# Performance work log

Hardware: AMD Instinct MI355X
Metric: run time of the kernel (lower is better)

Reference implementation:

```python
import jax, jax.numpy as jnp
import numpy as np

B = 16384
F = 128   # num_features
H = 128   # hidden_dim
E = 32    # embedding_dim


def setup_inputs() -> dict:
    key = jax.random.key(0)
    k_x, k_w1, k_b1, k_w2, k_b2 = jax.random.split(key, 5)
    # Per-feature params stacked along feature axis.
    # Layer 1: Linear(1 -> H): weight [F, H] (in_dim==1 squeezed), bias [F, H]
    # Layer 2: Linear(H -> E): weight [F, H, E], bias [F, E]
    # Torch default init: U(-1/sqrt(fan_in), 1/sqrt(fan_in))
    w1 = jax.random.uniform(k_w1, (F, H), jnp.float32, -1.0, 1.0)          # fan_in=1
    b1 = jax.random.uniform(k_b1, (F, H), jnp.float32, -1.0, 1.0)
    bound2 = 1.0 / np.sqrt(H)
    w2 = jax.random.uniform(k_w2, (F, H, E), jnp.float32, -bound2, bound2)
    b2 = jax.random.uniform(k_b2, (F, E), jnp.float32, -bound2, bound2)
    x = jax.random.normal(k_x, (B, F), jnp.float32)
    return {"x": x, "w1": w1, "b1": b1, "w2": w2, "b2": b2}


def reference(x, w1, b1, w2, b2):
    # Fused over features: broadcast-mul replaces K=1 matmuls,
    # single batched GEMM replaces per-feature second Linear.
    h = jax.nn.relu(x[:, :, None] * w1[None] + b1[None])   # [B, F, H]
    out = jnp.einsum('bfh,fhe->bfe', h, w2) + b2[None]      # [B, F, E]
    return out.reshape(x.shape[0], F * E)                   # concat along last dim
```

## Files before the change

### kernel.cpp

```cpp
#include <hip/hip_runtime.h>
#include <math.h>

#define B_N 16384
#define F_N 128
#define H_N 128
#define E_N 32
#define ROWS (H_N + 1)

typedef float f4v __attribute__((ext_vector_type(4)));

__global__ __launch_bounds__(128) void build_tables(
    const float* __restrict__ w1, const float* __restrict__ b1,
    const float* __restrict__ w2, const float* __restrict__ b2,
    float* __restrict__ ts_out, float* __restrict__ tab)
{
    __shared__ float w1s[H_N], b1s[H_N], ts[H_N];
    __shared__ int   hidx[H_N];
    __shared__ float w2s[H_N * E_N];
    __shared__ float dA[H_N * E_N];
    __shared__ float dC[H_N * E_N];
    __shared__ float baseA[4 * E_N], baseC[4 * E_N];
    __shared__ float gtA[4 * E_N], gtC[4 * E_N];

    const int f   = blockIdx.x;
    const int tid = threadIdx.x;

    float w1v = w1[f * H_N + tid];
    float b1v = b1[f * H_N + tid];
    w1s[tid] = w1v;
    b1s[tid] = b1v;
    ts[tid]   = (w1v != 0.0f) ? (-b1v / w1v) : INFINITY;
    hidx[tid] = tid;

    {
        const float4* src = (const float4*)(w2 + (size_t)f * H_N * E_N);
        float4*       dst = (float4*)w2s;
        #pragma unroll
        for (int it = 0; it < 8; ++it) dst[it * 128 + tid] = src[it * 128 + tid];
    }
    __syncthreads();

    for (int k = 2; k <= H_N; k <<= 1) {
        for (int j = k >> 1; j > 0; j >>= 1) {
            int ixj = tid ^ j;
            if (ixj > tid) {
                float a = ts[tid], bv = ts[ixj];
                bool up = ((tid & k) == 0);
                bool sw = up ? (a > bv) : (a < bv);
                if (sw) {
                    int ia = hidx[tid];
                    ts[tid] = bv; ts[ixj] = a;
                    hidx[tid] = hidx[ixj]; hidx[ixj] = ia;
                }
            }
            __syncthreads();
        }
    }

    ts_out[f * H_N + tid] = ts[tid];

    const int e = tid & 31;
    const int g = tid >> 5;

    #pragma unroll 4
    for (int jj = 0; jj < 32; ++jj) {
        int   j   = g * 32 + jj;
        int   p   = hidx[j];
        float w1h = w1s[p], b1h = b1s[p];
        float w2v = w2s[p * E_N + e];
        float s   = (w1h > 0.f) ? 1.f : ((w1h < 0.f) ? -1.f : 0.f);
        dA[j * E_N + e] = s * w1h * w2v;
        dC[j * E_N + e] = s * b1h * w2v;
    }
    {
        float pA = 0.f, pC = 0.f;
        #pragma unroll 4
        for (int hh = 0; hh < 32; ++hh) {
            int   h   = g * 32 + hh;
            float w1h = w1s[h], b1h = b1s[h];
            float w2v = w2s[h * E_N + e];
            if (w1h < 0.f) {
                pA = fmaf(w1h, w2v, pA);
                pC = fmaf(b1h, w2v, pC);
            } else if (w1h == 0.f && b1h > 0.f) {
                pC = fmaf(b1h, w2v, pC);
            }
        }
        baseA[g * E_N + e] = pA;
        baseC[g * E_N + e] = pC;
    }

    {
        float aA = 0.f, aC = 0.f;
        for (int jj = 0; jj < 32; ++jj) {
            int idx = (g * 32 + jj) * E_N + e;
            aA += dA[idx]; dA[idx] = aA;
            aC += dC[idx]; dC[idx] = aC;
        }
        gtA[g * E_N + e] = aA;
        gtC[g * E_N + e] = aC;
    }
    __syncthreads();

    float offA = baseA[e] + baseA[E_N + e] + baseA[2 * E_N + e] + baseA[3 * E_N + e];
    float offC = baseC[e] + baseC[E_N + e] + baseC[2 * E_N + e] + baseC[3 * E_N + e]
               + b2[f * E_N + e];
    for (int gg = 0; gg < g; ++gg) {
        offA += gtA[gg * E_N + e];
        offC += gtC[gg * E_N + e];
    }

    const size_t base = (size_t)f * ROWS * 64;
    if (g == 0) {
        tab[base + e]      = offA;
        tab[base + 32 + e] = offC;
    }
    #pragma unroll 4
    for (int jj = 0; jj < 32; ++jj) {
        int j = g * 32 + jj;
        tab[base + (size_t)(j + 1) * 64 + e]      = offA + dA[j * E_N + e];
        tab[base + (size_t)(j + 1) * 64 + 32 + e] = offC + dC[j * E_N + e];
    }
}

#define FH 32
#define NB 64

__global__ __launch_bounds__(256, 4) void apply_tables(
    const float* __restrict__ x, const float* __restrict__ ts,
    const float* __restrict__ tab, float* __restrict__ out)
{
    __shared__ float lds_t[FH * ROWS];
    __shared__ float xs[NB * FH];
    __shared__ int   los[NB * FH];

    const int tid = threadIdx.x;

    const unsigned bid  = blockIdx.x;
    const unsigned work = (bid & 7u) * 128u + (bid >> 3);
    const int b0 = (int)(work & 255u) * NB;
    const int f0 = (int)(work >> 8)  * FH;

    {
        const float4* src = (const float4*)(ts + (size_t)f0 * H_N);
        #pragma unroll
        for (int it = 0; it < 4; ++it) {
            int    vi  = it * 256 + tid;
            float4 v   = src[vi];
            int    idx = vi * 4;
            int    fl  = idx >> 7;
            int    j   = idx & 127;
            float* dst = &lds_t[fl * ROWS + j];
            dst[0] = v.x; dst[1] = v.y; dst[2] = v.z; dst[3] = v.w;
        }
    }
    {
        #pragma unroll
        for (int it = 0; it < 2; ++it) {
            int vi = it * 256 + tid;
            int bl = vi >> 3;
            int fq = (vi & 7) * 4;
            float4 v = *(const float4*)(x + (size_t)(b0 + bl) * F_N + f0 + fq);
            *(float4*)(&xs[bl * FH + fq]) = v;
        }
    }
    __syncthreads();

    {
        const int fa = tid & 31;
        const int rg = tid >> 5;
        const float* tloc = &lds_t[fa * ROWS];
        float xv[8];
        int   lo[8], hi[8];
        #pragma unroll
        for (int j = 0; j < 8; ++j) {
            xv[j] = xs[(rg * 8 + j) * FH + fa];
            lo[j] = 0; hi[j] = H_N;
        }
        #pragma unroll
        for (int s = 0; s < 7; ++s) {
            #pragma unroll
            for (int j = 0; j < 8; ++j) {
                int  mid = (lo[j] + hi[j]) >> 1;
                bool lt  = tloc[mid] < xv[j];
                lo[j] = lt ? mid + 1 : lo[j];
                hi[j] = lt ? hi[j] : mid;
            }
        }
        #pragma unroll
        for (int j = 0; j < 8; ++j) los[(rg * 8 + j) * FH + fa] = lo[j];
    }
    __syncthreads();

    const int fl = tid >> 3;
    const int eq = tid & 7;
    const int fg = f0 + fl;
    const float* tb = tab + (size_t)fg * ROWS * 64 + eq * 4;
    float*       op = out + (size_t)b0 * (F_N * E_N) + (size_t)fg * E_N + eq * 4;

    #pragma unroll 4
    for (int r = 0; r < NB; ++r) {
        int   lo = los[r * FH + fl];
        float xv = xs[r * FH + fl];
        const float* row = tb + (size_t)lo * 64;
        f4v a4 = *(const f4v*)(row);
        f4v c4 = *(const f4v*)(row + 32);
        f4v o;
        o.x = fmaf(xv, a4.x, c4.x);
        o.y = fmaf(xv, a4.y, c4.y);
        o.z = fmaf(xv, a4.z, c4.z);
        o.w = fmaf(xv, a4.w, c4.w);
        __builtin_nontemporal_store(o, (f4v*)(op + (size_t)r * (F_N * E_N)));
    }
}

__global__ __launch_bounds__(256) void direct_kernel(
    const float* __restrict__ x, const float* __restrict__ w1,
    const float* __restrict__ b1, const float* __restrict__ w2,
    const float* __restrict__ b2, float* __restrict__ out)
{
    __shared__ float w1s[H_N], b1s[H_N], b2s[E_N];
    __shared__ float w2s[H_N * E_N];
    const int f   = blockIdx.y;
    const int tid = threadIdx.x;
    if (tid < H_N) { w1s[tid] = w1[f * H_N + tid]; b1s[tid] = b1[f * H_N + tid]; }
    for (int i = tid; i < H_N * E_N; i += 256) w2s[i] = w2[(size_t)f * H_N * E_N + i];
    if (tid < E_N) b2s[tid] = b2[f * E_N + tid];
    __syncthreads();

    const int b  = blockIdx.x * 256 + tid;
    float xv = x[(size_t)b * F_N + f];
    float acc[E_N];
    #pragma unroll
    for (int e = 0; e < E_N; ++e) acc[e] = b2s[e];
    for (int h = 0; h < H_N; ++h) {
        float hv = fmaxf(fmaf(xv, w1s[h], b1s[h]), 0.f);
        #pragma unroll
        for (int e = 0; e < E_N; ++e) acc[e] = fmaf(hv, w2s[h * E_N + e], acc[e]);
    }
    float* op = out + (size_t)b * (F_N * E_N) + (size_t)f * E_N;
    #pragma unroll
    for (int e = 0; e < E_N; e += 4)
        *(float4*)(op + e) = make_float4(acc[e], acc[e + 1], acc[e + 2], acc[e + 3]);
}

extern "C" void kernel_launch(void* const* d_in, const int* in_sizes, int n_in,
                              void* d_out, int out_size, void* d_ws, size_t ws_size,
                              hipStream_t stream) {
    const float* x  = (const float*)d_in[0];
    const float* w1 = (const float*)d_in[1];
    const float* b1 = (const float*)d_in[2];
    const float* w2 = (const float*)d_in[3];
    const float* b2 = (const float*)d_in[4];
    float* out = (float*)d_out;

    const size_t n_ts  = (size_t)F_N * H_N;
    const size_t n_tab = (size_t)F_N * ROWS * 64;
    const size_t need  = (n_ts + n_tab) * sizeof(float);

    if (ws_size >= need) {
        float* ts  = (float*)d_ws;
        float* tab = ts + n_ts;
        build_tables<<<dim3(F_N), dim3(128), 0, stream>>>(w1, b1, w2, b2, ts, tab);
        apply_tables<<<dim3((B_N / NB) * (F_N / FH)), dim3(256), 0, stream>>>(x, ts, tab, out);
    } else {
        direct_kernel<<<dim3(B_N / 256, F_N), dim3(256), 0, stream>>>(x, w1, b1, w2, b2, out);
    }
}
```

Baseline: 287.7 us.

## Interleave A/C table rows, shuffle search results, halve batch tile

The table layout now interleaves A and C coefficients in groups of four, so each lane reads one contiguous 32-byte span instead of two separate 16-byte loads. apply_tables drops the shared x and segment-index buffers and one barrier. Each thread now binary-searches 4 rows itself and broadcasts the results with wave shuffles. The batch tile shrinks from 64 to 32 rows and occupancy is raised to 8 blocks. This trades LDS traffic and a sync for more blocks, a repeated ts load per block, and shuffle overhead.

```diff
diff --git a/kernel.cpp b/kernel.cpp
--- a/kernel.cpp
+++ b/kernel.cpp
@@ -8,6 +8,8 @@
 #define ROWS (H_N + 1)
 
 typedef float f4v __attribute__((ext_vector_type(4)));
+
+__device__ __forceinline__ int eidxA(int e) { return ((e >> 2) << 3) | (e & 3); }
 
 __global__ __launch_bounds__(128) void build_tables(
     const float* __restrict__ w1, const float* __restrict__ b1,
@@ -111,35 +113,34 @@
     }
 
     const size_t base = (size_t)f * ROWS * 64;
+    const int    eA   = eidxA(e);
     if (g == 0) {
-        tab[base + e]      = offA;
-        tab[base + 32 + e] = offC;
+        tab[base + eA]     = offA;
+        tab[base + eA + 4] = offC;
     }
     #pragma unroll 4
     for (int jj = 0; jj < 32; ++jj) {
         int j = g * 32 + jj;
-        tab[base + (size_t)(j + 1) * 64 + e]      = offA + dA[j * E_N + e];
-        tab[base + (size_t)(j + 1) * 64 + 32 + e] = offC + dC[j * E_N + e];
+        tab[base + (size_t)(j + 1) * 64 + eA]     = offA + dA[j * E_N + e];
+        tab[base + (size_t)(j + 1) * 64 + eA + 4] = offC + dC[j * E_N + e];
     }
 }
 
 #define FH 32
-#define NB 64
-
-__global__ __launch_bounds__(256, 4) void apply_tables(
+#define NB 32
+
+__global__ __launch_bounds__(256, 8) void apply_tables(
     const float* __restrict__ x, const float* __restrict__ ts,
     const float* __restrict__ tab, float* __restrict__ out)
 {
     __shared__ float lds_t[FH * ROWS];
-    __shared__ float xs[NB * FH];
-    __shared__ int   los[NB * FH];
 
     const int tid = threadIdx.x;
 
     const unsigned bid  = blockIdx.x;
-    const unsigned work = (bid & 7u) * 128u + (bid >> 3);
-    const int b0 = (int)(work & 255u) * NB;
-    const int f0 = (int)(work >> 8)  * FH;
+    const unsigned work = (bid & 7u) * 256u + (bid >> 3);
+    const int b0 = (int)(work & 511u) * NB;
+    const int f0 = (int)(work >> 9)  * FH;
 
     {
         const float4* src = (const float4*)(ts + (size_t)f0 * H_N);
@@ -148,69 +149,59 @@
             int    vi  = it * 256 + tid;
             float4 v   = src[vi];
             int    idx = vi * 4;
-            int    fl  = idx >> 7;
+            int    fl_ = idx >> 7;
             int    j   = idx & 127;
-            float* dst = &lds_t[fl * ROWS + j];
+            float* dst = &lds_t[fl_ * ROWS + j];
             dst[0] = v.x; dst[1] = v.y; dst[2] = v.z; dst[3] = v.w;
         }
     }
-    {
-        #pragma unroll
-        for (int it = 0; it < 2; ++it) {
-            int vi = it * 256 + tid;
-            int bl = vi >> 3;
-            int fq = (vi & 7) * 4;
-            float4 v = *(const float4*)(x + (size_t)(b0 + bl) * F_N + f0 + fq);
-            *(float4*)(&xs[bl * FH + fq]) = v;
-        }
-    }
-    __syncthreads();
-
-    {
-        const int fa = tid & 31;
-        const int rg = tid >> 5;
-        const float* tloc = &lds_t[fa * ROWS];
-        float xv[8];
-        int   lo[8], hi[8];
-        #pragma unroll
-        for (int j = 0; j < 8; ++j) {
-            xv[j] = xs[(rg * 8 + j) * FH + fa];
-            lo[j] = 0; hi[j] = H_N;
+    __syncthreads();
+
+    const int lane = tid & 63;
+    const int fl   = tid >> 3;
+    const int eq   = tid & 7;
+
+    float xv[4]; int lo4[4];
+    {
+        const float* tloc = &lds_t[fl * ROWS];
+        int hi4[4];
+        #pragma unroll
+        for (int j = 0; j < 4; ++j) {
+            xv[j]  = x[(size_t)(b0 + eq * 4 + j) * F_N + f0 + fl];
+            lo4[j] = 0; hi4[j] = H_N;
         }
         #pragma unroll
         for (int s = 0; s < 7; ++s) {
             #pragma unroll
-            for (int j = 0; j < 8; ++j) {
-                int  mid = (lo[j] + hi[j]) >> 1;
+            for (int j = 0; j < 4; ++j) {
+                int  mid = (lo4[j] + hi4[j]) >> 1;
                 bool lt  = tloc[mid] < xv[j];
-                lo[j] = lt ? mid + 1 : lo[j];
-                hi[j] = lt ? hi[j] : mid;
+                lo4[j] = lt ? mid + 1 : lo4[j];
+                hi4[j] = lt ? hi4[j] : mid;
             }
         }
-        #pragma unroll
-        for (int j = 0; j < 8; ++j) los[(rg * 8 + j) * FH + fa] = lo[j];
-    }
-    __syncthreads();
-
-    const int fl = tid >> 3;
-    const int eq = tid & 7;
-    const int fg = f0 + fl;
-    const float* tb = tab + (size_t)fg * ROWS * 64 + eq * 4;
-    float*       op = out + (size_t)b0 * (F_N * E_N) + (size_t)fg * E_N + eq * 4;
-
-    #pragma unroll 4
-    for (int r = 0; r < NB; ++r) {
-        int   lo = los[r * FH + fl];
-        float xv = xs[r * FH + fl];
-        const float* row = tb + (size_t)lo * 64;
-        f4v a4 = *(const f4v*)(row);
-        f4v c4 = *(const f4v*)(row + 32);
-        f4v o;
-        o.x = fmaf(xv, a4.x, c4.x);
-        o.y = fmaf(xv, a4.y, c4.y);
-        o.z = fmaf(xv, a4.z, c4.z);
-        o.w = fmaf(xv, a4.w, c4.w);
-        __builtin_nontemporal_store(o, (f4v*)(op + (size_t)r * (F_N * E_N)));
+    }
+
+    const float* tb = tab + (size_t)(f0 + fl) * ROWS * 64 + eq * 8;
+    float*       op = out + (size_t)b0 * (F_N * E_N) + (size_t)(f0 + fl) * E_N + eq * 4;
+    const int gbase = lane & 56;
+
+    for (int c = 0; c < 8; ++c) {
+        #pragma unroll
+        for (int j = 0; j < 4; ++j) {
+            int   r   = c * 4 + j;
+            int   lo  = __shfl(lo4[j], gbase | c);
+            float xvr = __shfl(xv[j],  gbase | c);
+            const float* row = tb + (size_t)lo * 64;
+            f4v a  = *(const f4v*)(row);
+            f4v cc = *(const f4v*)(row + 4);
+            f4v o;
+            o.x = fmaf(xvr, a.x, cc.x);
+            o.y = fmaf(xvr, a.y, cc.y);
+            o.z = fmaf(xvr, a.z, cc.z);
+            o.w = fmaf(xvr, a.w, cc.w);
+            __builtin_nontemporal_store(o, (f4v*)(op + (size_t)r * (F_N * E_N)));
+        }
     }
 }
 
```

Result: slower. 299.6 us (+4.1%).
